# Optimization experiments

Measured on AMD Instinct MI355X. Metric: run time of the kernel, lower is better.

## Reference

```python
import jax, jax.numpy as jnp
import numpy as np

N_HEADS = 16
D_K = 64
MAX_REL = 32


def setup_inputs() -> dict:
    key = jax.random.key(0)
    k1, k2, k3, k4 = jax.random.split(key, 4)
    B, T, D = 2, 2048, 1024
    x = jax.random.normal(k1, (B, T, D), dtype=jnp.float32)
    # torch nn.Linear weights are [out, in]; y = x @ W.T
    W_q = jax.random.normal(k2, (D, D), dtype=jnp.float32) / np.sqrt(D)
    W_o = jax.random.normal(k3, (D, D), dtype=jnp.float32) / np.sqrt(D)
    rel_k_emb = jax.random.normal(k4, (2 * MAX_REL + 1, D_K), dtype=jnp.float32)
    return {"x": x, "W_q": W_q, "W_o": W_o, "rel_k_emb": rel_k_emb}


def reference(x, W_q, W_o, rel_k_emb):
    B, T, D = x.shape
    H, dk = N_HEADS, D_K
    scale = 1.0 / np.sqrt(dk).astype(np.float32)
    # NOTE: source module (faithfully) uses W_q for q, k AND v.
    q = (x @ W_q.T).reshape(B, T, H, dk).transpose(0, 2, 1, 3)  # [B,H,T,dk]
    k = q
    v = q
    scores = jnp.einsum('bhid,bhjd->bhij', q, k) * scale  # [B,H,T,T]
    pos = jnp.arange(T)
    rel = jnp.clip(pos[:, None] - pos[None, :], -MAX_REL, MAX_REL) + MAX_REL  # [T,T]
    rel_keys = rel_k_emb[rel]  # [T,T,dk]
    rel_logits = jnp.einsum('bhid,ijd->bhij', q, rel_keys) * scale
    scores = scores + rel_logits
    attn = jax.nn.softmax(scores, axis=-1)
    out = jnp.einsum('bhij,bhjd->bhid', attn, v)  # [B,H,T,dk]
    out = out.transpose(0, 2, 1, 3).reshape(B, T, D)
    return out @ W_o.T
```

## Files before the change

### kernel.cpp

```cpp
#include <hip/hip_runtime.h>
#include <stdint.h>

typedef unsigned short u16;
typedef __attribute__((ext_vector_type(8))) short short8;
typedef __attribute__((ext_vector_type(4))) float f32x4;

#define MFMA16(a, b, c) __builtin_amdgcn_mfma_f32_16x16x32_bf16((a), (b), (c), 0, 0, 0)

__device__ __forceinline__ void gload16(const void* g, void* l) {
  __builtin_amdgcn_global_load_lds((const __attribute__((address_space(1))) void*)g,
                                   (__attribute__((address_space(3))) void*)l, 16, 0, 0);
}

__device__ __forceinline__ u16 bf16bits(float f) {
  union { float f; unsigned u; } x; x.f = f;
  unsigned r = x.u + 0x7fffu + ((x.u >> 16) & 1u);
  return (u16)(r >> 16);
}

__device__ __forceinline__ float bf16tof(u16 b) {
  union { unsigned u; float f; } x; x.u = ((unsigned)b) << 16;
  return x.f;
}

__device__ __forceinline__ float exp2fast(float x) {
  float r;
  asm("v_exp_f32 %0, %1" : "=v"(r) : "v"(x));
  return r;
}

__global__ __launch_bounds__(256) void cvt4(const float* __restrict__ s0, u16* __restrict__ d0, int n0,
                                            const float* __restrict__ s1, u16* __restrict__ d1, int n1,
                                            const float* __restrict__ s2, u16* __restrict__ d2, int n2,
                                            const float* __restrict__ s3, u16* __restrict__ d3, int n3) {
  const float* s; u16* d; int n;
  switch (blockIdx.y) {
    case 0:  s = s0; d = d0; n = n0; break;
    case 1:  s = s1; d = d1; n = n1; break;
    case 2:  s = s2; d = d2; n = n2; break;
    default: s = s3; d = d3; n = n3; break;
  }
  int stride = gridDim.x * blockDim.x;
  for (int i = blockIdx.x * blockDim.x + threadIdx.x; i * 8 < n; i += stride) {
    float4 a = ((const float4*)s)[i * 2];
    float4 b = ((const float4*)s)[i * 2 + 1];
    union { u16 u[8]; uint4 v; } pk;
    pk.u[0] = bf16bits(a.x); pk.u[1] = bf16bits(a.y);
    pk.u[2] = bf16bits(a.z); pk.u[3] = bf16bits(a.w);
    pk.u[4] = bf16bits(b.x); pk.u[5] = bf16bits(b.y);
    pk.u[6] = bf16bits(b.z); pk.u[7] = bf16bits(b.w);
    ((uint4*)d)[i] = pk.v;
  }
}

template <int EPI>
__global__ __launch_bounds__(512) void gemm_bt(const u16* __restrict__ A,
                                               const u16* __restrict__ Bw,
                                               u16* __restrict__ out0,
                                               u16* __restrict__ out1,
                                               float* __restrict__ outf,
                                               int M, int N, int K) {
  __shared__ __align__(16) char smem[2 * 16384];
  const int tid = threadIdx.x;
  const int lane = tid & 63, w = tid >> 6;
  const int g = lane >> 4, l15 = lane & 15;
  const int m0 = blockIdx.y * 128, n0 = blockIdx.x * 128;
  const int wm = w >> 2, wn = w & 3;
  const int NK = K >> 5;
  f32x4 acc[4][2] = {};

  auto stage = [&](int kk, int buf) {
    char* Ab_l = smem + buf * 16384;
    char* Bb_l = smem + buf * 16384 + 8192;
    int row = w * 16 + (lane >> 2);
    const char* Ab = (const char*)A + ((size_t)m0 * K + kk * 32) * 2;
    gload16(Ab + (size_t)row * (K * 2) + (lane & 3) * 16, Ab_l + w * 1024);
    const char* Bb = (const char*)Bw + ((size_t)n0 * K + kk * 32) * 2;
    gload16(Bb + (size_t)row * (K * 2) + (lane & 3) * 16, Bb_l + w * 1024);
  };

  stage(0, 0);
  __syncthreads();
  for (int kk = 0; kk < NK; ++kk) {
    int buf = kk & 1;
    if (kk + 1 < NK) stage(kk + 1, buf ^ 1);
    const char* Abuf = smem + buf * 16384;
    const char* Bbuf = Abuf + 8192;
    short8 af[4], bfr[2];
#pragma unroll
    for (int mt = 0; mt < 4; ++mt)
      af[mt] = *(const short8*)(Abuf + (wm * 64 + mt * 16 + l15) * 64 + g * 16);
#pragma unroll
    for (int nt = 0; nt < 2; ++nt)
      bfr[nt] = *(const short8*)(Bbuf + (wn * 32 + nt * 16 + l15) * 64 + g * 16);
#pragma unroll
    for (int mt = 0; mt < 4; ++mt)
#pragma unroll
      for (int nt = 0; nt < 2; ++nt)
        acc[mt][nt] = MFMA16(af[mt], bfr[nt], acc[mt][nt]);
    __syncthreads();
  }

#pragma unroll
  for (int mt = 0; mt < 4; ++mt)
#pragma unroll
    for (int nt = 0; nt < 2; ++nt) {
      int n = n0 + wn * 32 + nt * 16 + l15;
      int mbase = m0 + wm * 64 + mt * 16 + 4 * g;
      if constexpr (EPI == 0) {
#pragma unroll
        for (int r = 0; r < 4; ++r)
          outf[(size_t)(mbase + r) * N + n] = acc[mt][nt][r];
      } else {
        int b = mbase >> 11, t = mbase & 2047;
        int h = n >> 6, d = n & 63;
        size_t bhb = (size_t)(b * 16 + h) * (2048 * 64);
        union { u16 u[4]; uint2 v; } pk;
#pragma unroll
        for (int r = 0; r < 4; ++r) {
          u16 uu = bf16bits(acc[mt][nt][r]);
          out0[bhb + (size_t)(t + r) * 64 + d] = uu;
          pk.u[r] = uu;
        }
        *(uint2*)(out1 + bhb + (size_t)d * 2048 + t) = pk.v;
      }
    }
}

__global__ __launch_bounds__(256) void attn_rel(const u16* __restrict__ qtd,
                                                const u16* __restrict__ qdt,
                                                const u16* __restrict__ relk,
                                                u16* __restrict__ outa) {
  __shared__ __align__(16) char smem[49152];
  const int tid = threadIdx.x;
  const int lane = tid & 63, w = tid >> 6;
  const int g = lane >> 4, l15 = lane & 15;
  int lin = blockIdx.y * 32 + blockIdx.x;
  int sidx = lin >> 3;
  const int bh = (lin & 7) * 4 + (sidx & 3);
  const int q0 = (sidx >> 2) * 64;
  const int q0w = q0 + w * 16;
  u16* qrelb = (u16*)(smem + 32768);
  char* Pbuf = smem + 40960 + w * 2048;

  short8 qa[2];
  {
    size_t rowoff = ((size_t)bh * 2048 + q0w + l15) * 64;
    qa[0] = *(const short8*)(qtd + rowoff + g * 8);
    qa[1] = *(const short8*)(qtd + rowoff + g * 8 + 32);
    const float QS = 0.18033688f;
#pragma unroll
    for (int c = 0; c < 2; ++c)
#pragma unroll
      for (int e = 0; e < 8; ++e)
        qa[c][e] = (short)bf16bits(bf16tof((u16)qa[c][e]) * QS);
  }

  for (int c = tid; c < 520; c += 256)
    *(uint4*)(smem + c * 16) = *(const uint4*)((const char*)relk + c * 16);
  for (int c = 520 + tid; c < 640; c += 256) {
    uint4 z; z.x = 0u; z.y = 0u; z.z = 0u; z.w = 0u;
    *(uint4*)(smem + c * 16) = z;
  }
  __syncthreads();

  f32x4 aq[5] = {};
#pragma unroll
  for (int t = 0; t < 5; ++t)
#pragma unroll
    for (int c = 0; c < 2; ++c) {
      short8 rb = *(const short8*)(smem + ((t * 16 + l15) * 64 + g * 8 + c * 32) * 2);
      aq[t] = MFMA16(rb, qa[c], aq[t]);
    }
  float bhi = __shfl(aq[4][0], l15);
  float blo = __shfl(aq[0][0], l15);
#pragma unroll
  for (int t = 0; t < 4; ++t)
#pragma unroll
    for (int r = 0; r < 4; ++r)
      qrelb[(w * 16 + l15) * 64 + t * 16 + 4 * g + r] = bf16bits(aq[t][r]);
  __syncthreads();

  auto stageKV = [&](int kv0, int buf) {
    char* Kb = smem + buf * 16384;
    char* Vb = Kb + 8192;
    int sub = lane >> 3, chunk = lane & 7;
#pragma unroll
    for (int i = 0; i < 2; ++i) {
      int rloc = (w * 2 + i) * 8 + sub;
      int swz = (chunk * 16) ^ ((rloc & 7) << 4);
      gload16((const char*)qtd + ((size_t)bh * 2048 + kv0 + rloc) * 128 + swz,
              Kb + (w * 2 + i) * 1024);
      gload16((const char*)qdt + ((size_t)bh * 64 + rloc) * 4096 + kv0 * 2 + swz,
              Vb + (w * 2 + i) * 1024);
    }
  };

  f32x4 aco[4] = {};
  float lrow = 0.f;

  stageKV(0, 0);
  __syncthreads();
  for (int ti = 0; ti < 32; ++ti) {
    int buf = ti & 1;
    int kv0 = ti * 64;
    if (ti + 1 < 32) stageKV(kv0 + 64, buf ^ 1);
    const char* Kb = smem + buf * 16384;
    const char* Vb = Kb + 8192;

    f32x4 s[4];
    bool farL = (q0w - (kv0 + 63)) >= 32;
    bool farR = (q0w + 15 - kv0) <= -32;
    if (farL || farR) {
      float bv = farL ? bhi : blo;
      f32x4 binit = {bv, bv, bv, bv};
#pragma unroll
      for (int jt = 0; jt < 4; ++jt) s[jt] = binit;
    } else {
#pragma unroll
      for (int jt = 0; jt < 4; ++jt)
#pragma unroll
        for (int r = 0; r < 4; ++r) {
          int dd = (q0w + l15) - (kv0 + jt * 16 + 4 * g + r);
          int idx = dd < -32 ? 0 : (dd > 31 ? 63 : dd + 32);
          float tb = bf16tof(qrelb[(w * 16 + l15) * 64 + idx]);
          s[jt][r] = dd >= 32 ? bhi : tb;
        }
    }

#pragma unroll
    for (int jt = 0; jt < 4; ++jt) {
      int jloc = jt * 16 + l15;
      int sw = (jloc & 7) << 4;
#pragma unroll
      for (int c = 0; c < 2; ++c) {
        short8 kb = *(const short8*)(Kb + ((jloc * 128 + g * 16 + c * 64) ^ sw));
        s[jt] = MFMA16(kb, qa[c], s[jt]);
      }
    }

    float lsum = 0.f;
    int psw = (l15 & 7) << 4;
#pragma unroll
    for (int jt = 0; jt < 4; ++jt) {
      float p0 = exp2fast(s[jt][0]);
      float p1 = exp2fast(s[jt][1]);
      float p2 = exp2fast(s[jt][2]);
      float p3 = exp2fast(s[jt][3]);
      lsum += (p0 + p1) + (p2 + p3);
      union { float f; unsigned u; } c0, c1, c2, c3;
      c0.f = p0; c1.f = p1; c2.f = p2; c3.f = p3;
      uint2 wv;
      wv.x = (c0.u >> 16) | (c1.u & 0xFFFF0000u);
      wv.y = (c2.u >> 16) | (c3.u & 0xFFFF0000u);
      *(uint2*)(Pbuf + ((l15 * 128 + jt * 32 + g * 8) ^ psw)) = wv;
    }
    lrow += lsum;

    short8 pa0 = *(const short8*)(Pbuf + ((l15 * 128 + g * 16) ^ psw));
    short8 pa1 = *(const short8*)(Pbuf + ((l15 * 128 + g * 16 + 64) ^ psw));
#pragma unroll
    for (int dt = 0; dt < 4; ++dt) {
      int dloc = dt * 16 + l15;
      int sw = (dloc & 7) << 4;
      short8 vb0 = *(const short8*)(Vb + ((dloc * 128 + g * 16) ^ sw));
      short8 vb1 = *(const short8*)(Vb + ((dloc * 128 + g * 16 + 64) ^ sw));
      aco[dt] = MFMA16(pa0, vb0, aco[dt]);
      aco[dt] = MFMA16(pa1, vb1, aco[dt]);
    }
    __syncthreads();
  }

  lrow += __shfl_xor(lrow, 16);
  lrow += __shfl_xor(lrow, 32);

  int b = bh >> 4, h = bh & 15;
#pragma unroll
  for (int r = 0; r < 4; ++r) {
    float lr = __shfl(lrow, 4 * g + r);
    float rl = 1.0f / lr;
    int t = q0w + 4 * g + r;
    size_t base = ((size_t)(b * 2048 + t) * 16 + h) * 64;
#pragma unroll
    for (int dt = 0; dt < 4; ++dt)
      outa[base + dt * 16 + l15] = bf16bits(aco[dt][r] * rl);
  }
}

extern "C" void kernel_launch(void* const* d_in, const int* in_sizes, int n_in,
                              void* d_out, int out_size, void* d_ws, size_t ws_size,
                              hipStream_t stream) {
  const float* x    = (const float*)d_in[0];
  const float* Wq   = (const float*)d_in[1];
  const float* Wo   = (const float*)d_in[2];
  const float* relk = (const float*)d_in[3];
  float* out = (float*)d_out;

  u16* q_td   = (u16*)d_ws;
  u16* q_dt   = q_td + 4194304;
  u16* x_bf   = q_dt + 4194304;
  u16* wq_bf  = x_bf + 4194304;
  u16* wo_bf  = wq_bf + 1048576;
  u16* rel_bf = wo_bf + 1048576;
  u16* attn   = x_bf;

  cvt4<<<dim3(2048, 4), 256, 0, stream>>>(x, x_bf, 4194304,
                                          Wq, wq_bf, 1048576,
                                          Wo, wo_bf, 1048576,
                                          relk, rel_bf, 4160);
  gemm_bt<1><<<dim3(8, 32), 512, 0, stream>>>(x_bf, wq_bf, q_td, q_dt, nullptr,
                                              4096, 1024, 1024);
  attn_rel<<<dim3(32, 32), 256, 0, stream>>>(q_td, q_dt, rel_bf, attn);
  gemm_bt<0><<<dim3(8, 32), 512, 0, stream>>>(attn, wo_bf, nullptr, nullptr, out,
                                              4096, 1024, 1024);
}
```

Before: 119.3 us.

## Double GEMM k-tile to 64 and XOR-swizzle LDS layout

The projection GEMM now stages a 64-wide k slice per iteration instead of 32, which halves the number of barriers and loop iterations and doubles the LDS buffers to 64 KB. Global-to-LDS loads use an XOR swizzle on the 16-byte chunk index keyed by row, and the fragment reads apply the same swizzle to avoid LDS bank conflicts on the 128-byte row stride. The larger LDS footprint may reduce how many blocks fit per CU.

```diff
diff --git a/kernel.cpp b/kernel.cpp
--- a/kernel.cpp
+++ b/kernel.cpp
@@ -60,23 +60,29 @@
                                                u16* __restrict__ out1,
                                                float* __restrict__ outf,
                                                int M, int N, int K) {
-  __shared__ __align__(16) char smem[2 * 16384];
+  __shared__ __align__(16) char smem[2 * 32768];
   const int tid = threadIdx.x;
   const int lane = tid & 63, w = tid >> 6;
   const int g = lane >> 4, l15 = lane & 15;
   const int m0 = blockIdx.y * 128, n0 = blockIdx.x * 128;
   const int wm = w >> 2, wn = w & 3;
-  const int NK = K >> 5;
+  const int NK = K >> 6;
+  const size_t K2 = (size_t)K * 2;
   f32x4 acc[4][2] = {};
 
   auto stage = [&](int kk, int buf) {
-    char* Ab_l = smem + buf * 16384;
-    char* Bb_l = smem + buf * 16384 + 8192;
-    int row = w * 16 + (lane >> 2);
-    const char* Ab = (const char*)A + ((size_t)m0 * K + kk * 32) * 2;
-    gload16(Ab + (size_t)row * (K * 2) + (lane & 3) * 16, Ab_l + w * 1024);
-    const char* Bb = (const char*)Bw + ((size_t)n0 * K + kk * 32) * 2;
-    gload16(Bb + (size_t)row * (K * 2) + (lane & 3) * 16, Bb_l + w * 1024);
+    char* Ab_l = smem + buf * 32768;
+    char* Bb_l = smem + buf * 32768 + 16384;
+    int sub = lane >> 3, chunk = lane & 7;
+    const char* Ab = (const char*)A + ((size_t)m0 * K + kk * 64) * 2;
+    const char* Bb = (const char*)Bw + ((size_t)n0 * K + kk * 64) * 2;
+#pragma unroll
+    for (int i = 0; i < 2; ++i) {
+      int row = i * 64 + w * 8 + sub;
+      int swz = (chunk * 16) ^ ((row & 7) << 4);
+      gload16(Ab + (size_t)row * K2 + swz, Ab_l + i * 8192 + w * 1024);
+      gload16(Bb + (size_t)row * K2 + swz, Bb_l + i * 8192 + w * 1024);
+    }
   };
 
   stage(0, 0);
@@ -84,20 +90,31 @@
   for (int kk = 0; kk < NK; ++kk) {
     int buf = kk & 1;
     if (kk + 1 < NK) stage(kk + 1, buf ^ 1);
-    const char* Abuf = smem + buf * 16384;
-    const char* Bbuf = Abuf + 8192;
-    short8 af[4], bfr[2];
-#pragma unroll
-    for (int mt = 0; mt < 4; ++mt)
-      af[mt] = *(const short8*)(Abuf + (wm * 64 + mt * 16 + l15) * 64 + g * 16);
-#pragma unroll
-    for (int nt = 0; nt < 2; ++nt)
-      bfr[nt] = *(const short8*)(Bbuf + (wn * 32 + nt * 16 + l15) * 64 + g * 16);
-#pragma unroll
-    for (int mt = 0; mt < 4; ++mt)
-#pragma unroll
-      for (int nt = 0; nt < 2; ++nt)
-        acc[mt][nt] = MFMA16(af[mt], bfr[nt], acc[mt][nt]);
+    const char* Abuf = smem + buf * 32768;
+    const char* Bbuf = Abuf + 16384;
+    int sw = (l15 & 7) << 4;
+    short8 af[4][2], bfr[2][2];
+#pragma unroll
+    for (int mt = 0; mt < 4; ++mt) {
+      int row = wm * 64 + mt * 16 + l15;
+#pragma unroll
+      for (int c = 0; c < 2; ++c)
+        af[mt][c] = *(const short8*)(Abuf + ((row * 128 + g * 16 + c * 64) ^ sw));
+    }
+#pragma unroll
+    for (int nt = 0; nt < 2; ++nt) {
+      int row = wn * 32 + nt * 16 + l15;
+#pragma unroll
+      for (int c = 0; c < 2; ++c)
+        bfr[nt][c] = *(const short8*)(Bbuf + ((row * 128 + g * 16 + c * 64) ^ sw));
+    }
+#pragma unroll
+    for (int c = 0; c < 2; ++c)
+#pragma unroll
+      for (int mt = 0; mt < 4; ++mt)
+#pragma unroll
+        for (int nt = 0; nt < 2; ++nt)
+          acc[mt][nt] = MFMA16(af[mt][c], bfr[nt][c], acc[mt][nt]);
     __syncthreads();
   }
 
```

Result: faster. 115.5 us (-3.3%).
